# Optimization experiments

Measured on AMD Instinct MI355X. Metric: run time of the kernel, lower is better.

The kernel has to match this reference:

```python
import jax, jax.numpy as jnp
import numpy as np

N_NODES = 100000
N_EDGES = 1600000
IN_FEATS = 128
H_FEATS = 64
NUM_CLASSES = 16


def setup_inputs() -> dict:
    key = jax.random.key(0)
    ks = jax.random.split(key, 6)
    X = jax.random.normal(ks[0], (N_NODES, IN_FEATS), dtype=jnp.float32)
    edge_weight = jax.random.uniform(ks[1], (N_EDGES,), dtype=jnp.float32)
    W1 = jax.random.normal(ks[2], (IN_FEATS, H_FEATS), dtype=jnp.float32) * (1.0 / np.sqrt(IN_FEATS))
    b1 = jnp.zeros((H_FEATS,), dtype=jnp.float32)
    W2 = jax.random.normal(ks[3], (H_FEATS, NUM_CLASSES), dtype=jnp.float32) * (1.0 / np.sqrt(H_FEATS))
    b2 = jnp.zeros((NUM_CLASSES,), dtype=jnp.float32)
    edge_src = jax.random.randint(ks[4], (N_EDGES,), 0, N_NODES, dtype=jnp.int32)
    edge_dst = jax.random.randint(ks[5], (N_EDGES,), 0, N_NODES, dtype=jnp.int32)
    return {"X": X, "edge_weight": edge_weight, "W1": W1, "b1": b1,
            "W2": W2, "b2": b2, "edge_src": edge_src, "edge_dst": edge_dst}


def _gcn_conv(H, W, b, edge_src, edge_dst, edge_weight, num_nodes):
    # transform-then-aggregate: out = A @ (H @ W) + b, A given as weighted edge list
    H = H @ W                                  # [N, d_out]
    msgs = H[edge_src] * edge_weight[:, None]  # [E, d_out] gather + scale
    agg = jax.ops.segment_sum(msgs, edge_dst, num_segments=num_nodes)  # scatter-add
    return agg + b


def reference(X, edge_weight, W1, b1, W2, b2, edge_src, edge_dst):
    n = X.shape[0]
    h = jax.nn.relu(_gcn_conv(X, W1, b1, edge_src, edge_dst, edge_weight, n))
    return _gcn_conv(h, W2, b2, edge_src, edge_dst, edge_weight, n)
```

## Files before the change

kernel.cpp:

```cpp
#include <hip/hip_runtime.h>

#define N_NODES 100000
#define N_EDGES 1600000
#define IN_F 128
#define H_F 64
#define C_F 16

#define BIN_SH 7
#define BIN_NODES 128
#define NBINS 782
#define BCAP 2816
#define PART_BLOCKS 196
#define GEMM1_BLOCKS 1563
#define RMAX 6
#define AGG_STRIDE 36

typedef __attribute__((ext_vector_type(8))) short bf16x8;
typedef __attribute__((ext_vector_type(4))) float f32x4;

__device__ inline unsigned short f2bf(float f) {
  unsigned u = __float_as_uint(f);
  unsigned r = (u + 0x7fff + ((u >> 16) & 1)) >> 16;
  return (unsigned short)r;
}

__global__ __launch_bounds__(256) void part_gemm1_kernel(
    const int* __restrict__ src, const int* __restrict__ dst,
    const float* __restrict__ ew, int* __restrict__ binCnt,
    int2* __restrict__ ebin, const float* __restrict__ X,
    const float* __restrict__ W1, unsigned short* __restrict__ H1b) {
  __shared__ char ldsraw[16 * 1024];
  int tid = threadIdx.x;
  if (blockIdx.x < PART_BLOCKS) {
    int* hist = (int*)ldsraw;
    int* base = hist + NBINS;
    for (int i = tid; i < NBINS; i += 256) hist[i] = 0;
    __syncthreads();
    int i0 = blockIdx.x * 2048;
    int iHi = i0 + 2048;
    if (iHi > N_EDGES / 4) iHi = N_EDGES / 4;
    const int4* d4p = (const int4*)dst;
    const int4* s4p = (const int4*)src;
    const float4* w4p = (const float4*)ew;
    unsigned key[32];
    unsigned aux[32];
#pragma unroll
    for (int it = 0; it < 8; ++it) {
      int i = i0 + it * 256 + tid;
      if (i < iHi) {
        int4 d = d4p[i];
        int4 s = s4p[i];
        float4 w = w4p[i];
#pragma unroll
        for (int j = 0; j < 4; ++j) {
          int dd = (&d.x)[j];
          int ss = (&s.x)[j];
          float ww = (&w.x)[j];
          int bb = dd >> BIN_SH;
          unsigned wf = (unsigned)(ww * 32767.0f + 0.5f);
          key[it * 4 + j] =
              (unsigned)ss | ((unsigned)(dd & (BIN_NODES - 1)) << 17);
          aux[it * 4 + j] = wf | ((unsigned)bb << 15);
          atomicAdd(&hist[bb], 1);
        }
      }
    }
    __syncthreads();
    for (int i = tid; i < NBINS; i += 256)
      base[i] = hist[i] ? atomicAdd(&binCnt[i], hist[i]) : 0;
    __syncthreads();
#pragma unroll
    for (int it = 0; it < 8; ++it) {
      int i = i0 + it * 256 + tid;
      if (i < iHi) {
        int pos[4];
#pragma unroll
        for (int j = 0; j < 4; ++j)
          pos[j] = atomicAdd(&base[aux[it * 4 + j] >> 15], 1);
#pragma unroll
        for (int j = 0; j < 4; ++j) {
          unsigned a = aux[it * 4 + j];
          ebin[(size_t)(a >> 15) * BCAP + pos[j]] =
              make_int2((int)key[it * 4 + j], (int)(a & 0x7FFF));
        }
      }
    }
  } else {
    short* ldsB = (short*)ldsraw;
    for (int idx = tid; idx < 16 * 512; idx += 256) {
      int frag = idx >> 9;
      int entry = idx & 511;
      int lane = entry >> 3, j = entry & 7;
      int c = frag >> 2, s = frag & 3;
      int k = s * 32 + (lane >> 4) * 8 + j;
      int n = c * 16 + (lane & 15);
      ldsB[idx] = (short)f2bf(W1[k * H_F + n]);
    }
    __syncthreads();
    int wave = tid >> 6;
    int lane = tid & 63;
    int rt = (blockIdx.x - PART_BLOCKS) * 4 + wave;
    if (rt >= N_NODES / 16) return;
    int node0 = rt * 16;
    int l = lane & 15, q = lane >> 4;
    const float* xp = X + (size_t)(node0 + l) * IN_F + q * 8;
    f32x4 acc[4] = {f32x4{0.f, 0.f, 0.f, 0.f}, f32x4{0.f, 0.f, 0.f, 0.f},
                    f32x4{0.f, 0.f, 0.f, 0.f}, f32x4{0.f, 0.f, 0.f, 0.f}};
#pragma unroll
    for (int s = 0; s < 4; ++s) {
      float4 x0 = *(const float4*)(xp + s * 32);
      float4 x1 = *(const float4*)(xp + s * 32 + 4);
      bf16x8 a;
      a[0] = f2bf(x0.x); a[1] = f2bf(x0.y); a[2] = f2bf(x0.z); a[3] = f2bf(x0.w);
      a[4] = f2bf(x1.x); a[5] = f2bf(x1.y); a[6] = f2bf(x1.z); a[7] = f2bf(x1.w);
#pragma unroll
      for (int c = 0; c < 4; ++c) {
        bf16x8 b = *(const bf16x8*)&ldsB[(c * 4 + s) * 512 + lane * 8];
        acc[c] = __builtin_amdgcn_mfma_f32_16x16x32_bf16(a, b, acc[c], 0, 0, 0);
      }
    }
#pragma unroll
    for (int c = 0; c < 4; ++c)
#pragma unroll
      for (int r = 0; r < 4; ++r)
        H1b[(size_t)(node0 + q * 4 + r) * H_F + c * 16 + l] = f2bf(acc[c][r]);
  }
}

__global__ __launch_bounds__(512) void gather1f_kernel(
    const uint2* __restrict__ H1q, const int* __restrict__ binCnt,
    int2* __restrict__ ebin, int2* __restrict__ segB,
    const float* __restrict__ b1, const float* __restrict__ W2,
    unsigned short* __restrict__ H2b) {
  __shared__ int h[BIN_NODES], sc[BIN_NODES], cur[BIN_NODES];
  __shared__ unsigned srt[BCAP];
  __shared__ unsigned aggU[BIN_NODES * AGG_STRIDE];
  __shared__ short ldsW2[2 * 512];
  int b = blockIdx.x, tid = threadIdx.x;
  for (int idx = tid; idx < 1024; idx += 512) {
    int sfrag = idx >> 9;
    int entry = idx & 511;
    int lane = entry >> 3, j = entry & 7;
    int k = sfrag * 32 + (lane >> 4) * 8 + j;
    int c = lane & 15;
    ldsW2[idx] = (short)f2bf(W2[k * C_F + c]);
  }
  int lo = b * BCAP;
  int cnt = binCnt[b];
  if (tid < BIN_NODES) h[tid] = 0;
  __syncthreads();
  unsigned rk[RMAX];
  int rd[RMAX];
  int rn = 0;
#pragma unroll
  for (int j = 0; j < RMAX; ++j) {
    int e = j * 512 + tid;
    if (e < cnt) {
      int2 r = ebin[lo + e];
      int dl = (((unsigned)r.x) >> 17) & (BIN_NODES - 1);
      rk[j] = ((unsigned)r.x & 0x1FFFF) | ((unsigned)r.y << 17);
      rd[j] = dl;
      atomicAdd(&h[dl], 1);
      rn = j + 1;
    }
  }
  __syncthreads();
  if (tid < BIN_NODES) sc[tid] = h[tid];
  __syncthreads();
#pragma unroll
  for (int d = 1; d < BIN_NODES; d <<= 1) {
    int t = 0;
    if (tid < BIN_NODES && tid >= d) t = sc[tid - d];
    __syncthreads();
    if (tid < BIN_NODES) sc[tid] += t;
    __syncthreads();
  }
  if (tid < BIN_NODES) cur[tid] = sc[tid] - h[tid];
  __syncthreads();
#pragma unroll
  for (int j = 0; j < RMAX; ++j)
    if (j < rn) {
      int pos = atomicAdd(&cur[rd[j]], 1);
      srt[pos] = rk[j];
    }
  __syncthreads();
  {
    unsigned* ebinU = (unsigned*)ebin;
    int lo2 = lo << 1;
    for (int i = tid; i < cnt; i += 512) ebinU[lo2 + i] = srt[i];
    if (tid < BIN_NODES) {
      int n = (b << BIN_SH) + tid;
      if (n < N_NODES) segB[n] = make_int2(sc[tid] - h[tid], sc[tid]);
    }
  }
  int wv = tid >> 6, lane = tid & 63, g = lane >> 4, li = lane & 15;
  const float wsc = 1.0f / 32767.0f;
  float bb0 = b1[li * 4], bb1 = b1[li * 4 + 1];
  float bb2 = b1[li * 4 + 2], bb3 = b1[li * 4 + 3];
  for (int k = 0; k < 16; ++k) {
    int nl = wv * 16 + k;
    int n = (b << BIN_SH) + nl;
    if (n >= N_NODES) break;
    int e1 = sc[nl], e0 = e1 - h[nl];
    f32x4 a0 = {0.f, 0.f, 0.f, 0.f}, a1 = {0.f, 0.f, 0.f, 0.f};
    f32x4 a2 = {0.f, 0.f, 0.f, 0.f}, a3 = {0.f, 0.f, 0.f, 0.f};
    int i = e0;
    for (; i + 15 < e1; i += 16) {
      unsigned r0 = srt[i + g];
      unsigned r1 = srt[i + 4 + g];
      unsigned r2 = srt[i + 8 + g];
      unsigned r3 = srt[i + 12 + g];
      uint2 v0 = H1q[(r0 & 0x1FFFF) * (H_F / 4) + li];
      uint2 v1 = H1q[(r1 & 0x1FFFF) * (H_F / 4) + li];
      uint2 v2 = H1q[(r2 & 0x1FFFF) * (H_F / 4) + li];
      uint2 v3 = H1q[(r3 & 0x1FFFF) * (H_F / 4) + li];
      float w0 = (float)(r0 >> 17) * wsc, w1 = (float)(r1 >> 17) * wsc;
      float w2 = (float)(r2 >> 17) * wsc, w3 = (float)(r3 >> 17) * wsc;
      a0[0] += __uint_as_float(v0.x << 16) * w0;
      a0[1] += __uint_as_float(v0.x & 0xFFFF0000u) * w0;
      a0[2] += __uint_as_float(v0.y << 16) * w0;
      a0[3] += __uint_as_float(v0.y & 0xFFFF0000u) * w0;
      a1[0] += __uint_as_float(v1.x << 16) * w1;
      a1[1] += __uint_as_float(v1.x & 0xFFFF0000u) * w1;
      a1[2] += __uint_as_float(v1.y << 16) * w1;
      a1[3] += __uint_as_float(v1.y & 0xFFFF0000u) * w1;
      a2[0] += __uint_as_float(v2.x << 16) * w2;
      a2[1] += __uint_as_float(v2.x & 0xFFFF0000u) * w2;
      a2[2] += __uint_as_float(v2.y << 16) * w2;
      a2[3] += __uint_as_float(v2.y & 0xFFFF0000u) * w2;
      a3[0] += __uint_as_float(v3.x << 16) * w3;
      a3[1] += __uint_as_float(v3.x & 0xFFFF0000u) * w3;
      a3[2] += __uint_as_float(v3.y << 16) * w3;
      a3[3] += __uint_as_float(v3.y & 0xFFFF0000u) * w3;
    }
    for (; i + 3 < e1; i += 4) {
      unsigned r0 = srt[i + g];
      uint2 v0 = H1q[(r0 & 0x1FFFF) * (H_F / 4) + li];
      float w0 = (float)(r0 >> 17) * wsc;
      a0[0] += __uint_as_float(v0.x << 16) * w0;
      a0[1] += __uint_as_float(v0.x & 0xFFFF0000u) * w0;
      a0[2] += __uint_as_float(v0.y << 16) * w0;
      a0[3] += __uint_as_float(v0.y & 0xFFFF0000u) * w0;
    }
    if (i + g < e1) {
      unsigned r0 = srt[i + g];
      uint2 v0 = H1q[(r0 & 0x1FFFF) * (H_F / 4) + li];
      float w0 = (float)(r0 >> 17) * wsc;
      a1[0] += __uint_as_float(v0.x << 16) * w0;
      a1[1] += __uint_as_float(v0.x & 0xFFFF0000u) * w0;
      a1[2] += __uint_as_float(v0.y << 16) * w0;
      a1[3] += __uint_as_float(v0.y & 0xFFFF0000u) * w0;
    }
    f32x4 a = (a0 + a1) + (a2 + a3);
#pragma unroll
    for (int c = 0; c < 4; ++c) {
      a[c] += __shfl_xor(a[c], 16, 64);
      a[c] += __shfl_xor(a[c], 32, 64);
    }
    if (g == 0) {
      float r0 = fmaxf(a[0] + bb0, 0.f);
      float r1 = fmaxf(a[1] + bb1, 0.f);
      float r2 = fmaxf(a[2] + bb2, 0.f);
      float r3 = fmaxf(a[3] + bb3, 0.f);
      unsigned p0 = (unsigned)f2bf(r0) | ((unsigned)f2bf(r1) << 16);
      unsigned p1 = (unsigned)f2bf(r2) | ((unsigned)f2bf(r3) << 16);
      *(uint2*)&aggU[nl * AGG_STRIDE + li * 2] = make_uint2(p0, p1);
    }
  }
  __syncthreads();
  int l = lane & 15, q = lane >> 4;
  int nl0 = wv * 16;
  f32x4 acc = {0.f, 0.f, 0.f, 0.f};
#pragma unroll
  for (int s = 0; s < 2; ++s) {
    bf16x8 afr = *(const bf16x8*)&aggU[(nl0 + l) * AGG_STRIDE + s * 16 + q * 4];
    bf16x8 bfr = *(const bf16x8*)&ldsW2[s * 512 + lane * 8];
    acc = __builtin_amdgcn_mfma_f32_16x16x32_bf16(afr, bfr, acc, 0, 0, 0);
  }
  int node0 = (b << BIN_SH) + nl0;
#pragma unroll
  for (int r = 0; r < 4; ++r) {
    int n = node0 + q * 4 + r;
    if (n < N_NODES) H2b[(size_t)n * C_F + l] = f2bf(acc[r]);
  }
}

__global__ __launch_bounds__(512) void gather2s_kernel(
    const uint2* __restrict__ H2q, const int* __restrict__ binCnt,
    const int2* __restrict__ ebin, const int2* __restrict__ segB,
    const float* __restrict__ b2, float* __restrict__ out) {
  __shared__ int2 segl[BIN_NODES];
  __shared__ unsigned srt[BCAP];
  int b = blockIdx.x, tid = threadIdx.x;
  int cnt = binCnt[b];
  const unsigned* ebinU = (const unsigned*)ebin;
  int lo2 = (b * BCAP) << 1;
  for (int i = tid; i < cnt; i += 512) srt[i] = ebinU[lo2 + i];
  if (tid < BIN_NODES) {
    int n = (b << BIN_SH) + tid;
    segl[tid] = (n < N_NODES) ? segB[n] : make_int2(0, 0);
  }
  __syncthreads();
  int wv = tid >> 6, lane = tid & 63, g = lane >> 2, li = lane & 3;
  const float wsc = 1.0f / 32767.0f;
  float bb0 = b2[li * 4], bb1 = b2[li * 4 + 1];
  float bb2 = b2[li * 4 + 2], bb3 = b2[li * 4 + 3];
  for (int k = 0; k < 16; ++k) {
    int nl = wv * 16 + k;
    int n = (b << BIN_SH) + nl;
    if (n >= N_NODES) break;
    int2 sgl = segl[nl];
    int e0 = sgl.x, e1 = sgl.y;
    f32x4 a0 = {0.f, 0.f, 0.f, 0.f};
    int i = e0;
    for (; i + 15 < e1; i += 16) {
      unsigned r0 = srt[i + g];
      uint2 v0 = H2q[(r0 & 0x1FFFF) * (C_F / 4) + li];
      float w0 = (float)(r0 >> 17) * wsc;
      a0[0] += __uint_as_float(v0.x << 16) * w0;
      a0[1] += __uint_as_float(v0.x & 0xFFFF0000u) * w0;
      a0[2] += __uint_as_float(v0.y << 16) * w0;
      a0[3] += __uint_as_float(v0.y & 0xFFFF0000u) * w0;
    }
    if (i + g < e1) {
      unsigned r0 = srt[i + g];
      uint2 v0 = H2q[(r0 & 0x1FFFF) * (C_F / 4) + li];
      float w0 = (float)(r0 >> 17) * wsc;
      a0[0] += __uint_as_float(v0.x << 16) * w0;
      a0[1] += __uint_as_float(v0.x & 0xFFFF0000u) * w0;
      a0[2] += __uint_as_float(v0.y << 16) * w0;
      a0[3] += __uint_as_float(v0.y & 0xFFFF0000u) * w0;
    }
#pragma unroll
    for (int c = 0; c < 4; ++c) {
      a0[c] += __shfl_xor(a0[c], 4, 64);
      a0[c] += __shfl_xor(a0[c], 8, 64);
      a0[c] += __shfl_xor(a0[c], 16, 64);
      a0[c] += __shfl_xor(a0[c], 32, 64);
    }
    if (g == 0) {
      float4 o;
      o.x = a0[0] + bb0;
      o.y = a0[1] + bb1;
      o.z = a0[2] + bb2;
      o.w = a0[3] + bb3;
      *(float4*)&out[(size_t)n * C_F + li * 4] = o;
    }
  }
}

extern "C" void kernel_launch(void* const* d_in, const int* in_sizes, int n_in,
                              void* d_out, int out_size, void* d_ws,
                              size_t ws_size, hipStream_t stream) {
  const float* X  = (const float*)d_in[0];
  const float* ew = (const float*)d_in[1];
  const float* W1 = (const float*)d_in[2];
  const float* b1 = (const float*)d_in[3];
  const float* W2 = (const float*)d_in[4];
  const float* b2 = (const float*)d_in[5];
  const int* src  = (const int*)d_in[6];
  const int* dst  = (const int*)d_in[7];
  float* out = (float*)d_out;

  unsigned short* H1b = (unsigned short*)d_ws;
  unsigned short* H2b = H1b + (size_t)N_NODES * H_F;
  int2* ebin  = (int2*)(H2b + (size_t)N_NODES * C_F);
  int* binCnt = (int*)(ebin + (size_t)NBINS * BCAP);
  int2* segB  = (int2*)(binCnt + NBINS);

  hipMemsetAsync(binCnt, 0, NBINS * sizeof(int), stream);
  part_gemm1_kernel<<<PART_BLOCKS + GEMM1_BLOCKS, 256, 0, stream>>>(
      src, dst, ew, binCnt, ebin, X, W1, H1b);
  gather1f_kernel<<<NBINS, 512, 0, stream>>>((const uint2*)H1b, binCnt, ebin,
                                             segB, b1, W2, H2b);
  gather2s_kernel<<<NBINS, 512, 0, stream>>>((const uint2*)H2b, binCnt, ebin,
                                             segB, b2, out);
}
```

Before: 202.3 us.

## Replace global bin atomics with per-block local partition and offset table

The partition blocks now sort their edges locally by destination bin into a contiguous per-block region. They record per-block bin offsets in a table, which replaces global atomic bin counters and the memset. The gather1 kernel collects each bin's edges from 196 small slices using the offset table, then writes a compact sorted list that gather2 reads. This removes global atomics and scattered 8-byte bin writes, and packs records into 4 bytes plus a 1-byte destination. In exchange, gather1 must do many short, poorly coalesced slice reads done serially by a few threads each, twice.

Result: slower. 217.7 us (+7.6%).

```diff
diff --git a/kernel.cpp b/kernel.cpp
--- a/kernel.cpp
+++ b/kernel.cpp
@@ -11,8 +11,8 @@
 #define NBINS 782
 #define BCAP 2816
 #define PART_BLOCKS 196
+#define PBE 8192
 #define GEMM1_BLOCKS 1563
-#define RMAX 6
 #define AGG_STRIDE 36
 
 typedef __attribute__((ext_vector_type(8))) short bf16x8;
@@ -26,24 +26,26 @@
 
 __global__ __launch_bounds__(256) void part_gemm1_kernel(
     const int* __restrict__ src, const int* __restrict__ dst,
-    const float* __restrict__ ew, int* __restrict__ binCnt,
-    int2* __restrict__ ebin, const float* __restrict__ X,
-    const float* __restrict__ W1, unsigned short* __restrict__ H1b) {
+    const float* __restrict__ ew, unsigned* __restrict__ rec4,
+    unsigned char* __restrict__ dl1, int* __restrict__ offT,
+    const float* __restrict__ X, const float* __restrict__ W1,
+    unsigned short* __restrict__ H1b) {
   __shared__ char ldsraw[16 * 1024];
   int tid = threadIdx.x;
   if (blockIdx.x < PART_BLOCKS) {
     int* hist = (int*)ldsraw;
-    int* base = hist + NBINS;
-    for (int i = tid; i < NBINS; i += 256) hist[i] = 0;
-    __syncthreads();
-    int i0 = blockIdx.x * 2048;
-    int iHi = i0 + 2048;
+    int* cur = hist + 784;
+    int* part = cur + 782;
+    for (int i = tid; i < 784; i += 256) hist[i] = 0;
+    __syncthreads();
+    int i0 = blockIdx.x * (PBE / 4);
+    int iHi = i0 + (PBE / 4);
     if (iHi > N_EDGES / 4) iHi = N_EDGES / 4;
     const int4* d4p = (const int4*)dst;
     const int4* s4p = (const int4*)src;
     const float4* w4p = (const float4*)ew;
-    unsigned key[32];
-    unsigned aux[32];
+    unsigned r4[32];
+    int dd32[32];
 #pragma unroll
     for (int it = 0; it < 8; ++it) {
       int i = i0 + it * 256 + tid;
@@ -56,18 +58,50 @@
           int dd = (&d.x)[j];
           int ss = (&s.x)[j];
           float ww = (&w.x)[j];
-          int bb = dd >> BIN_SH;
           unsigned wf = (unsigned)(ww * 32767.0f + 0.5f);
-          key[it * 4 + j] =
-              (unsigned)ss | ((unsigned)(dd & (BIN_NODES - 1)) << 17);
-          aux[it * 4 + j] = wf | ((unsigned)bb << 15);
-          atomicAdd(&hist[bb], 1);
+          r4[it * 4 + j] = (unsigned)ss | (wf << 17);
+          dd32[it * 4 + j] = dd;
+          atomicAdd(&hist[dd >> BIN_SH], 1);
         }
       }
     }
     __syncthreads();
-    for (int i = tid; i < NBINS; i += 256)
-      base[i] = hist[i] ? atomicAdd(&binCnt[i], hist[i]) : 0;
+    int sl1 = 0, sl2 = 0, sl3 = 0;
+    if (tid < 196) {
+      int b0 = tid * 4;
+      int v0 = hist[b0], v1 = hist[b0 + 1], v2 = hist[b0 + 2],
+          v3 = hist[b0 + 3];
+      sl1 = v0;
+      sl2 = v0 + v1;
+      sl3 = v0 + v1 + v2;
+      part[tid] = v0 + v1 + v2 + v3;
+    }
+    __syncthreads();
+    for (int d = 1; d < 196; d <<= 1) {
+      int t = 0;
+      if (tid < 196 && tid >= d) t = part[tid - d];
+      __syncthreads();
+      if (tid < 196) part[tid] += t;
+      __syncthreads();
+    }
+    int blkBase = blockIdx.x * PBE;
+    if (tid < 196) {
+      int base0 = tid ? part[tid - 1] : 0;
+      int b0 = tid * 4;
+      int* op = offT + blockIdx.x * 783;
+      cur[b0] = base0;
+      op[b0] = blkBase + base0;
+      cur[b0 + 1] = base0 + sl1;
+      op[b0 + 1] = blkBase + base0 + sl1;
+      if (b0 + 2 < NBINS) {
+        cur[b0 + 2] = base0 + sl2;
+        op[b0 + 2] = blkBase + base0 + sl2;
+        cur[b0 + 3] = base0 + sl3;
+        op[b0 + 3] = blkBase + base0 + sl3;
+      }
+    }
+    if (tid == 0)
+      offT[blockIdx.x * 783 + 782] = blkBase + (iHi - i0) * 4;
     __syncthreads();
 #pragma unroll
     for (int it = 0; it < 8; ++it) {
@@ -76,12 +110,12 @@
         int pos[4];
 #pragma unroll
         for (int j = 0; j < 4; ++j)
-          pos[j] = atomicAdd(&base[aux[it * 4 + j] >> 15], 1);
+          pos[j] = atomicAdd(&cur[dd32[it * 4 + j] >> BIN_SH], 1);
 #pragma unroll
         for (int j = 0; j < 4; ++j) {
-          unsigned a = aux[it * 4 + j];
-          ebin[(size_t)(a >> 15) * BCAP + pos[j]] =
-              make_int2((int)key[it * 4 + j], (int)(a & 0x7FFF));
+          int g = blkBase + pos[j];
+          rec4[g] = r4[it * 4 + j];
+          dl1[g] = (unsigned char)(dd32[it * 4 + j] & (BIN_NODES - 1));
         }
       }
     }
@@ -128,11 +162,13 @@
 }
 
 __global__ __launch_bounds__(512) void gather1f_kernel(
-    const uint2* __restrict__ H1q, const int* __restrict__ binCnt,
-    int2* __restrict__ ebin, int2* __restrict__ segB,
+    const uint2* __restrict__ H1q, const unsigned* __restrict__ rec4,
+    const unsigned char* __restrict__ dl1, const int* __restrict__ offT,
+    unsigned* __restrict__ srtG, int2* __restrict__ segB,
     const float* __restrict__ b1, const float* __restrict__ W2,
     unsigned short* __restrict__ H2b) {
   __shared__ int h[BIN_NODES], sc[BIN_NODES], cur[BIN_NODES];
+  __shared__ int sS[196], sE[196];
   __shared__ unsigned srt[BCAP];
   __shared__ unsigned aggU[BIN_NODES * AGG_STRIDE];
   __shared__ short ldsW2[2 * 512];
@@ -145,24 +181,15 @@
     int c = lane & 15;
     ldsW2[idx] = (short)f2bf(W2[k * C_F + c]);
   }
-  int lo = b * BCAP;
-  int cnt = binCnt[b];
+  if (tid < 196) {
+    sS[tid] = offT[tid * 783 + b];
+    sE[tid] = offT[tid * 783 + b + 1];
+  }
   if (tid < BIN_NODES) h[tid] = 0;
   __syncthreads();
-  unsigned rk[RMAX];
-  int rd[RMAX];
-  int rn = 0;
-#pragma unroll
-  for (int j = 0; j < RMAX; ++j) {
-    int e = j * 512 + tid;
-    if (e < cnt) {
-      int2 r = ebin[lo + e];
-      int dl = (((unsigned)r.x) >> 17) & (BIN_NODES - 1);
-      rk[j] = ((unsigned)r.x & 0x1FFFF) | ((unsigned)r.y << 17);
-      rd[j] = dl;
-      atomicAdd(&h[dl], 1);
-      rn = j + 1;
-    }
+  if (tid < 392) {
+    int sl = tid >> 1, sub = tid & 1;
+    for (int i = sS[sl] + sub; i < sE[sl]; i += 2) atomicAdd(&h[dl1[i]], 1);
   }
   __syncthreads();
   if (tid < BIN_NODES) sc[tid] = h[tid];
@@ -177,17 +204,18 @@
   }
   if (tid < BIN_NODES) cur[tid] = sc[tid] - h[tid];
   __syncthreads();
-#pragma unroll
-  for (int j = 0; j < RMAX; ++j)
-    if (j < rn) {
-      int pos = atomicAdd(&cur[rd[j]], 1);
-      srt[pos] = rk[j];
-    }
+  if (tid < 392) {
+    int sl = tid >> 1, sub = tid & 1;
+    for (int i = sS[sl] + sub; i < sE[sl]; i += 2) {
+      int dl = dl1[i];
+      int pos = atomicAdd(&cur[dl], 1);
+      srt[pos] = rec4[i];
+    }
+  }
   __syncthreads();
   {
-    unsigned* ebinU = (unsigned*)ebin;
-    int lo2 = lo << 1;
-    for (int i = tid; i < cnt; i += 512) ebinU[lo2 + i] = srt[i];
+    int total = sc[BIN_NODES - 1];
+    for (int i = tid; i < total; i += 512) srtG[(size_t)b * BCAP + i] = srt[i];
     if (tid < BIN_NODES) {
       int n = (b << BIN_SH) + tid;
       if (n < N_NODES) segB[n] = make_int2(sc[tid] - h[tid], sc[tid]);
@@ -286,20 +314,25 @@
 }
 
 __global__ __launch_bounds__(512) void gather2s_kernel(
-    const uint2* __restrict__ H2q, const int* __restrict__ binCnt,
-    const int2* __restrict__ ebin, const int2* __restrict__ segB,
-    const float* __restrict__ b2, float* __restrict__ out) {
+    const uint2* __restrict__ H2q, const unsigned* __restrict__ srtG,
+    const int2* __restrict__ segB, const float* __restrict__ b2,
+    float* __restrict__ out) {
   __shared__ int2 segl[BIN_NODES];
   __shared__ unsigned srt[BCAP];
+  __shared__ int scnt;
   int b = blockIdx.x, tid = threadIdx.x;
-  int cnt = binCnt[b];
-  const unsigned* ebinU = (const unsigned*)ebin;
-  int lo2 = (b * BCAP) << 1;
-  for (int i = tid; i < cnt; i += 512) srt[i] = ebinU[lo2 + i];
   if (tid < BIN_NODES) {
     int n = (b << BIN_SH) + tid;
     segl[tid] = (n < N_NODES) ? segB[n] : make_int2(0, 0);
   }
+  if (tid == 0) {
+    int lastv = (b << BIN_SH) + BIN_NODES - 1;
+    if (lastv >= N_NODES) lastv = N_NODES - 1;
+    scnt = segB[lastv].y;
+  }
+  __syncthreads();
+  int cnt = scnt;
+  for (int i = tid; i < cnt; i += 512) srt[i] = srtG[(size_t)b * BCAP + i];
   __syncthreads();
   int wv = tid >> 6, lane = tid & 63, g = lane >> 2, li = lane & 3;
   const float wsc = 1.0f / 32767.0f;
@@ -364,15 +397,16 @@
 
   unsigned short* H1b = (unsigned short*)d_ws;
   unsigned short* H2b = H1b + (size_t)N_NODES * H_F;
-  int2* ebin  = (int2*)(H2b + (size_t)N_NODES * C_F);
-  int* binCnt = (int*)(ebin + (size_t)NBINS * BCAP);
-  int2* segB  = (int2*)(binCnt + NBINS);
-
-  hipMemsetAsync(binCnt, 0, NBINS * sizeof(int), stream);
+  unsigned* rec4 = (unsigned*)(H2b + (size_t)N_NODES * C_F);
+  unsigned char* dl1 = (unsigned char*)(rec4 + (size_t)PART_BLOCKS * PBE);
+  int* offT = (int*)(dl1 + (size_t)PART_BLOCKS * PBE);
+  unsigned* srtG = (unsigned*)(offT + PART_BLOCKS * 783);
+  int2* segB = (int2*)(srtG + (size_t)NBINS * BCAP);
+
   part_gemm1_kernel<<<PART_BLOCKS + GEMM1_BLOCKS, 256, 0, stream>>>(
-      src, dst, ew, binCnt, ebin, X, W1, H1b);
-  gather1f_kernel<<<NBINS, 512, 0, stream>>>((const uint2*)H1b, binCnt, ebin,
-                                             segB, b1, W2, H2b);
-  gather2s_kernel<<<NBINS, 512, 0, stream>>>((const uint2*)H2b, binCnt, ebin,
-                                             segB, b2, out);
+      src, dst, ew, rec4, dl1, offT, X, W1, H1b);
+  gather1f_kernel<<<NBINS, 512, 0, stream>>>((const uint2*)H1b, rec4, dl1,
+                                             offT, srtG, segB, b1, W2, H2b);
+  gather2s_kernel<<<NBINS, 512, 0, stream>>>((const uint2*)H2b, srtG, segB, b2,
+                                             out);
 }
```
